# Optimization experiments

Hardware: AMD Instinct MI355X
Metric: run time of the kernel (lower is better)

## Reference

```python
import jax, jax.numpy as jnp
import numpy as np

HIDDEN = 512
NUM_HEADS = 4
EPS = 1e-12  # torch F.normalize eps


def setup_inputs() -> dict:
    key = jax.random.key(0)
    k1, k2, k3, k4 = jax.random.split(key, 4)
    B, N, C = 4, 8192, HIDDEN
    x = jax.random.normal(k1, (B, N, C), dtype=jnp.float32)
    # nn.Linear weights: stored as [out_features, in_features]
    s = 1.0 / np.sqrt(C)
    W_qkv = jax.random.uniform(k2, (3 * C, C), dtype=jnp.float32, minval=-s, maxval=s)
    W_out = jax.random.uniform(k3, (C, C), dtype=jnp.float32, minval=-s, maxval=s)
    b_out = jax.random.uniform(k4, (C,), dtype=jnp.float32, minval=-s, maxval=s)
    temperature = jnp.ones((NUM_HEADS, 1, 1), dtype=jnp.float32)
    return {
        "x": x, "W_qkv": W_qkv, "W_out": W_out, "b_out": b_out,
        "temperature": temperature,
        "B_in": B, "C_in": C, "H": 32, "W": 32, "D": 8,
    }


def _l2norm(t):
    # F.normalize(t, dim=-1): t / max(||t||_2, eps)
    n = jnp.sqrt(jnp.sum(t * t, axis=-1, keepdims=True))
    return t / jnp.maximum(n, EPS)


def reference(x, W_qkv, W_out, b_out, temperature, B_in, C_in, H, W, D):
    B, N, C = x.shape
    h = NUM_HEADS
    dh = C // h
    # qkv: [B, N, 3C] -> [3, B, h, N, dh]
    qkv = (x @ W_qkv.T).reshape(B, N, 3, h, dh).transpose(2, 0, 3, 1, 4)
    q, k, v = qkv[0], qkv[1], qkv[2]
    # transpose to channel-major: [B, h, dh, N]
    q = jnp.swapaxes(q, -2, -1)
    k = jnp.swapaxes(k, -2, -1)
    v = jnp.swapaxes(v, -2, -1)
    q = _l2norm(q)
    k = _l2norm(k)
    # cross-covariance attention over channels: [B, h, dh, dh]
    attn = jnp.einsum('bhcn,bhdn->bhcd', q, k) * temperature
    attn = jax.nn.softmax(attn, axis=-1)
    # [B, h, dh, N] -> [B, N, h, dh] -> [B, N, C]
    x_ca = jnp.einsum('bhcd,bhdn->bhcn', attn, v)
    x_ca = x_ca.transpose(0, 3, 1, 2).reshape(B, N, C)
    return x_ca @ W_out.T + b_out
```

## Files before the change

kernel.cpp:

```cpp
#include <hip/hip_runtime.h>


typedef unsigned short ushort_t;
typedef __attribute__((ext_vector_type(8))) short short8;
typedef __attribute__((ext_vector_type(4))) float float4v;
typedef __attribute__((ext_vector_type(4))) unsigned short ushort4v;

__device__ __forceinline__ float bf2f(ushort_t b) {
  union { unsigned u; float f; } c; c.u = ((unsigned)b) << 16; return c.f;
}
__device__ __forceinline__ ushort_t f2bf(float f) {
  union { float f; unsigned u; } c; c.f = f;
  unsigned u = c.u;
  u += 0x7fffu + ((u >> 16) & 1u);
  return (ushort_t)(u >> 16);
}

typedef const __attribute__((address_space(1))) unsigned int guint_t;
typedef __attribute__((address_space(3))) unsigned int luint_t;
__device__ __forceinline__ void gl_lds16(const ushort_t* g, ushort_t* l) {
  __builtin_amdgcn_global_load_lds((guint_t*)g, (luint_t*)l, 16, 0, 0);
}

__global__ __launch_bounds__(256) void convert_bf16(
    const float* __restrict__ x, const float* __restrict__ w1,
    const float* __restrict__ w2, ushort_t* __restrict__ xb,
    ushort_t* __restrict__ w1b, ushort_t* __restrict__ w2b) {
  int g = blockIdx.x * 256 + threadIdx.x;
  const float* src; ushort_t* dst; int off;
  if (g < 4194304)      { src = x;  dst = xb;  off = g; }
  else if (g < 4390912) { src = w1; dst = w1b; off = g - 4194304; }
  else                  { src = w2; dst = w2b; off = g - 4390912; }
  size_t e = (size_t)off * 4;
  float4v f = *(const float4v*)(src + e);
  ushort4v o;
#pragma unroll
  for (int i = 0; i < 4; ++i) o[i] = f2bf(f[i]);
  *(ushort4v*)(dst + e) = o;
}

template <int MODE>
__global__ __launch_bounds__(256) void gemm128(
    const ushort_t* __restrict__ A, const ushort_t* __restrict__ B,
    float* __restrict__ outF, ushort_t* __restrict__ outU,
    ushort_t* __restrict__ q_ws, ushort_t* __restrict__ k_ws,
    ushort_t* __restrict__ v_tok, const float* __restrict__ bias) {
  const int tid = threadIdx.x;
  const int z = blockIdx.z;
  const int n0 = blockIdx.x * 128;
  const int m0 = blockIdx.y * 128;

  int lda, ldb, K;
  const ushort_t *Ab, *Bb;
  if constexpr (MODE == 0) { lda = 512; ldb = 512; K = 512; Ab = A; Bb = B; }
  else if constexpr (MODE == 1) {
    int bh = z >> 3, s = z & 7;
    lda = 8192; ldb = 8192; K = 1024;
    Ab = A + (size_t)bh * 1048576 + s * 1024;
    Bb = B + (size_t)bh * 1048576 + s * 1024;
  } else if constexpr (MODE == 2) {
    lda = 512; ldb = 128; K = 128;
    Ab = A + (z & 3) * 128;
    Bb = B + (size_t)z * 16384;
  } else {
    lda = 512; ldb = 512; K = 512;
    Ab = A + (size_t)z * 8192 * 512;
    Bb = B + (size_t)z * 512 * 512;
  }

  __shared__ ushort_t sA[128 * 64];
  __shared__ ushort_t sB[128 * 64];

  const int lr = tid >> 3;
  const int lc = (tid & 7) * 8;
  const ushort_t* ga = Ab + (size_t)(m0 + lr) * lda + lc;
  const ushort_t* gb = Bb + (size_t)(n0 + lr) * ldb + lc;
  ushort_t* la = &sA[lr * 64 + lc];
  ushort_t* lb = &sB[lr * 64 + lc];
  const size_t aStep = (size_t)32 * lda;
  const size_t bStep = (size_t)32 * ldb;

  const int w = tid >> 6;
  const int lane = tid & 63;
  const int l15 = lane & 15;
  const int quad = lane >> 4;
  const int wm = (w >> 1) * 64, wn = (w & 1) * 64;

  float4v acc[4][4];
#pragma unroll
  for (int i = 0; i < 4; ++i)
#pragma unroll
    for (int j = 0; j < 4; ++j) acc[i][j] = (float4v){0.f, 0.f, 0.f, 0.f};

  for (int kk = 0; kk < K; kk += 64) {
    __syncthreads();
#pragma unroll
    for (int i = 0; i < 4; ++i) {
      gl_lds16(ga + i * aStep + kk, la + i * 2048);
      gl_lds16(gb + i * bStep + kk, lb + i * 2048);
    }
    __syncthreads();
#pragma unroll
    for (int k2 = 0; k2 < 64; k2 += 32) {
      short8 af[4], bfr[4];
#pragma unroll
      for (int i = 0; i < 4; ++i)
        af[i] = *(const short8*)&sA[(wm + i * 16 + l15) * 64 + k2 + quad * 8];
#pragma unroll
      for (int j = 0; j < 4; ++j)
        bfr[j] = *(const short8*)&sB[(wn + j * 16 + l15) * 64 + k2 + quad * 8];
#pragma unroll
      for (int i = 0; i < 4; ++i)
#pragma unroll
        for (int j = 0; j < 4; ++j)
          acc[i][j] = __builtin_amdgcn_mfma_f32_16x16x32_bf16(af[i], bfr[j], acc[i][j], 0, 0, 0);
    }
  }

  if constexpr (MODE == 0) {
    const int t3 = n0 >> 9;
    const int h = (n0 >> 7) & 3;
    if (t3 == 2) {
#pragma unroll
      for (int i = 0; i < 4; ++i)
#pragma unroll
        for (int j = 0; j < 4; ++j) {
          int col = wn + j * 16 + l15;
#pragma unroll
          for (int rg = 0; rg < 4; ++rg) {
            int gr = m0 + wm + i * 16 + quad * 4 + rg;
            int b = gr >> 13, n = gr & 8191;
            v_tok[((size_t)b * 8192 + n) * 512 + h * 128 + col] = f2bf(acc[i][j][rg]);
          }
        }
    } else {
      ushort_t* dstT = t3 ? k_ws : q_ws;
#pragma unroll
      for (int i = 0; i < 4; ++i) {
        int gr = m0 + wm + i * 16 + quad * 4;
        int b = gr >> 13, n = gr & 8191;
        int bh = b * 4 + h;
#pragma unroll
        for (int j = 0; j < 4; ++j) {
          ushort4v pk;
#pragma unroll
          for (int rg = 0; rg < 4; ++rg) pk[rg] = f2bf(acc[i][j][rg]);
          *(ushort4v*)(dstT + ((size_t)bh * 128 + (wn + j * 16 + l15)) * 8192 + n) = pk;
        }
      }
    }
  } else if constexpr (MODE == 1) {
#pragma unroll
    for (int i = 0; i < 4; ++i)
#pragma unroll
      for (int j = 0; j < 4; ++j)
#pragma unroll
        for (int rg = 0; rg < 4; ++rg)
          outF[(size_t)z * 16384 + (size_t)(wm + i * 16 + quad * 4 + rg) * 128 +
               wn + j * 16 + l15] = acc[i][j][rg];
  } else if constexpr (MODE == 2) {
    int b = z >> 2, h = z & 3;
#pragma unroll
    for (int i = 0; i < 4; ++i)
#pragma unroll
      for (int j = 0; j < 4; ++j)
#pragma unroll
        for (int rg = 0; rg < 4; ++rg)
          outU[((size_t)b * 512 + m0 + wm + i * 16 + quad * 4 + rg) * 512 +
               h * 128 + wn + j * 16 + l15] = f2bf(acc[i][j][rg]);
  } else {
#pragma unroll
    for (int i = 0; i < 4; ++i)
#pragma unroll
      for (int j = 0; j < 4; ++j) {
        int gcol = n0 + wn + j * 16 + l15;
        float bv = bias[gcol];
#pragma unroll
        for (int rg = 0; rg < 4; ++rg)
          outF[((size_t)z * 8192 + m0 + wm + i * 16 + quad * 4 + rg) * 512 + gcol] =
              acc[i][j][rg] + bv;
      }
  }
}

__global__ __launch_bounds__(256) void norms_kernel(
    const ushort_t* __restrict__ q, const ushort_t* __restrict__ k,
    float* __restrict__ norms) {
  int w = threadIdx.x >> 6, lane = threadIdx.x & 63;
  int idx = blockIdx.x * 4 + w;
  const ushort_t* p = ((idx >> 11) ? k : q) + (size_t)(idx & 2047) * 8192;
  float s = 0.f;
#pragma unroll
  for (int it = 0; it < 16; ++it) {
    short8 v = *(const short8*)(p + (size_t)(it * 64 + lane) * 8);
#pragma unroll
    for (int e = 0; e < 8; ++e) {
      float f = bf2f((ushort_t)v[e]);
      s += f * f;
    }
  }
#pragma unroll
  for (int off = 32; off; off >>= 1) s += __shfl_xor(s, off);
  if (lane == 0) norms[idx] = sqrtf(s);
}

__global__ void attn_softmax(const float* __restrict__ Sp,
                             const float* __restrict__ norms,
                             const float* __restrict__ temp,
                             ushort_t* __restrict__ attn_t) {
  int c = blockIdx.x, bh = blockIdx.y, h = bh & 3;
  int lane = threadIdx.x;
  const float* base = Sp + (size_t)bh * 8 * 16384 + (size_t)c * 128;
  float v0 = 0.f, v1 = 0.f;
#pragma unroll
  for (int s = 0; s < 8; ++s) {
    v0 += base[s * 16384 + lane];
    v1 += base[s * 16384 + lane + 64];
  }
  float nq = fmaxf(norms[bh * 128 + c], 1e-12f);
  float sc = temp[h] / nq;
  v0 = v0 * sc / fmaxf(norms[2048 + bh * 128 + lane], 1e-12f);
  v1 = v1 * sc / fmaxf(norms[2048 + bh * 128 + lane + 64], 1e-12f);
  float m = fmaxf(v0, v1);
#pragma unroll
  for (int off = 32; off; off >>= 1) m = fmaxf(m, __shfl_xor(m, off));
  float e0 = expf(v0 - m), e1 = expf(v1 - m);
  float s = e0 + e1;
#pragma unroll
  for (int off = 32; off; off >>= 1) s += __shfl_xor(s, off);
  float inv = 1.0f / s;
  attn_t[(size_t)bh * 16384 + (size_t)lane * 128 + c] = f2bf(e0 * inv);
  attn_t[(size_t)bh * 16384 + (size_t)(lane + 64) * 128 + c] = f2bf(e1 * inv);
}

extern "C" void kernel_launch(void* const* d_in, const int* in_sizes, int n_in,
                              void* d_out, int out_size, void* d_ws, size_t ws_size,
                              hipStream_t stream) {
  const float* x    = (const float*)d_in[0];
  const float* Wqkv = (const float*)d_in[1];
  const float* Wout = (const float*)d_in[2];
  const float* bout = (const float*)d_in[3];
  const float* temp = (const float*)d_in[4];
  float* out = (float*)d_out;

  char* ws = (char*)d_ws;
  ushort_t* x_bf  = (ushort_t*)(ws);
  float*    S_par = (float*)(ws);
  float*    norms = (float*)(ws + 8388608);
  ushort_t* attnT = (ushort_t*)(ws + 8404992);
  ushort_t* W2b   = (ushort_t*)(ws + 8929280);
  ushort_t* q_ws  = (ushort_t*)(ws + 33554432);
  ushort_t* k_ws  = (ushort_t*)(ws + 67108864);
  ushort_t* v_tok = (ushort_t*)(ws + 100663296);
  ushort_t* Wqkvb = (ushort_t*)(ws + 134217728);
  ushort_t* Woutb = (ushort_t*)(ws + 135790592);

  convert_bf16<<<dim3(17408), dim3(256), 0, stream>>>(x, Wqkv, Wout, x_bf, Wqkvb, Woutb);

  gemm128<0><<<dim3(12, 256, 1), dim3(256), 0, stream>>>(
      x_bf, Wqkvb, nullptr, nullptr, q_ws, k_ws, v_tok, nullptr);

  norms_kernel<<<dim3(1024), dim3(256), 0, stream>>>(q_ws, k_ws, norms);

  gemm128<1><<<dim3(1, 1, 128), dim3(256), 0, stream>>>(
      q_ws, k_ws, S_par, nullptr, nullptr, nullptr, nullptr, nullptr);

  attn_softmax<<<dim3(128, 16), dim3(64), 0, stream>>>(S_par, norms, temp, attnT);

  gemm128<2><<<dim3(1, 4, 16), dim3(256), 0, stream>>>(
      Woutb, attnT, nullptr, W2b, nullptr, nullptr, nullptr, nullptr);

  gemm128<3><<<dim3(4, 64, 4), dim3(256), 0, stream>>>(
      v_tok, W2b, out, nullptr, nullptr, nullptr, nullptr, bout);
}
```

Before: 302.7 us.

## Fuse x bf16 conversion and norm computation into QKV GEMM, remap grids for XCD locality

Drops the separate fp32-to-bf16 conversion of x and instead converts it in registers inside a new QKV GEMM kernel, with register prefetch of the next K slice. The squared L2 norms of q and k are accumulated in the GEMM epilogue with atomics, replacing the standalone norms kernel. V output uses a swapped MFMA operand order so token-major stores are vectorized. The split-K for the Gram GEMM doubles to 16 splits, and the QKV and output GEMMs use 1D grids remapped so blocks are grouped by XCD. In exchange it adds a memset, float atomics that make norm summation order nondeterministic, and more register pressure.

```diff
diff --git a/kernel.cpp b/kernel.cpp
--- a/kernel.cpp
+++ b/kernel.cpp
@@ -22,68 +22,195 @@
   __builtin_amdgcn_global_load_lds((guint_t*)g, (luint_t*)l, 16, 0, 0);
 }
 
-__global__ __launch_bounds__(256) void convert_bf16(
-    const float* __restrict__ x, const float* __restrict__ w1,
-    const float* __restrict__ w2, ushort_t* __restrict__ xb,
+__global__ __launch_bounds__(256) void convert_w(
+    const float* __restrict__ w1, const float* __restrict__ w2,
     ushort_t* __restrict__ w1b, ushort_t* __restrict__ w2b) {
   int g = blockIdx.x * 256 + threadIdx.x;
   const float* src; ushort_t* dst; int off;
-  if (g < 4194304)      { src = x;  dst = xb;  off = g; }
-  else if (g < 4390912) { src = w1; dst = w1b; off = g - 4194304; }
-  else                  { src = w2; dst = w2b; off = g - 4390912; }
+  if (g < 196608) { src = w1; dst = w1b; off = g; }
+  else            { src = w2; dst = w2b; off = g - 196608; }
   size_t e = (size_t)off * 4;
   float4v f = *(const float4v*)(src + e);
   ushort4v o;
 #pragma unroll
   for (int i = 0; i < 4; ++i) o[i] = f2bf(f[i]);
   *(ushort4v*)(dst + e) = o;
+}
+
+template <bool SWAP>
+__device__ __forceinline__ void qkv_kloop(
+    const float* ga, const ushort_t* gb, ushort_t* la, ushort_t* lb,
+    const ushort_t* sA, const ushort_t* sB,
+    float4v (&acc)[4][4], int wm, int wn, int l15, int quad) {
+  float4v a0[4], a1[4];
+#pragma unroll
+  for (int i = 0; i < 4; ++i) {
+    a0[i] = *(const float4v*)(ga + i * 16384);
+    a1[i] = *(const float4v*)(ga + i * 16384 + 4);
+  }
+#pragma unroll
+  for (int kk = 0; kk < 512; kk += 64) {
+    __syncthreads();
+#pragma unroll
+    for (int i = 0; i < 4; ++i) {
+      short8 cv;
+#pragma unroll
+      for (int e = 0; e < 4; ++e) {
+        cv[e]     = (short)f2bf(a0[i][e]);
+        cv[e + 4] = (short)f2bf(a1[i][e]);
+      }
+      *(short8*)(la + i * 2048) = cv;
+      gl_lds16(gb + i * 16384 + kk, lb + i * 2048);
+    }
+    __syncthreads();
+    if (kk < 448) {
+#pragma unroll
+      for (int i = 0; i < 4; ++i) {
+        a0[i] = *(const float4v*)(ga + i * 16384 + kk + 64);
+        a1[i] = *(const float4v*)(ga + i * 16384 + kk + 68);
+      }
+    }
+#pragma unroll
+    for (int k2 = 0; k2 < 64; k2 += 32) {
+      short8 af[4], bfr[4];
+#pragma unroll
+      for (int i = 0; i < 4; ++i)
+        af[i] = *(const short8*)&sA[(wm + i * 16 + l15) * 64 + k2 + quad * 8];
+#pragma unroll
+      for (int j = 0; j < 4; ++j)
+        bfr[j] = *(const short8*)&sB[(wn + j * 16 + l15) * 64 + k2 + quad * 8];
+#pragma unroll
+      for (int i = 0; i < 4; ++i)
+#pragma unroll
+        for (int j = 0; j < 4; ++j) {
+          if constexpr (SWAP)
+            acc[i][j] = __builtin_amdgcn_mfma_f32_16x16x32_bf16(bfr[j], af[i], acc[i][j], 0, 0, 0);
+          else
+            acc[i][j] = __builtin_amdgcn_mfma_f32_16x16x32_bf16(af[i], bfr[j], acc[i][j], 0, 0, 0);
+        }
+    }
+  }
+}
+
+__global__ __launch_bounds__(256) void qkv_kernel(
+    const float* __restrict__ x, const ushort_t* __restrict__ Wb,
+    ushort_t* __restrict__ q_ws, ushort_t* __restrict__ k_ws,
+    ushort_t* __restrict__ v_tok, float* __restrict__ normsSq) {
+  const int l = blockIdx.x;
+  const int xcd = l & 7, lx = l >> 3;
+  const int col = lx % 12;
+  const int mrow = xcd * 32 + lx / 12;
+  const int n0 = col * 128, m0 = mrow * 128;
+
+  __shared__ ushort_t sA[8192];
+  __shared__ ushort_t sB[8192];
+
+  const int tid = threadIdx.x;
+  const int lr = tid >> 3, lc = (tid & 7) * 8;
+  const float* ga = x + (size_t)(m0 + lr) * 512 + lc;
+  const ushort_t* gb = Wb + (size_t)(n0 + lr) * 512 + lc;
+  ushort_t* la = &sA[lr * 64 + lc];
+  ushort_t* lb = &sB[lr * 64 + lc];
+
+  const int w = tid >> 6, lane = tid & 63, l15 = lane & 15, quad = lane >> 4;
+  const int wm = (w >> 1) * 64, wn = (w & 1) * 64;
+
+  float4v acc[4][4];
+#pragma unroll
+  for (int i = 0; i < 4; ++i)
+#pragma unroll
+    for (int j = 0; j < 4; ++j) acc[i][j] = (float4v){0.f, 0.f, 0.f, 0.f};
+
+  const bool isV = (n0 >= 1024);
+  if (isV) qkv_kloop<true>(ga, gb, la, lb, sA, sB, acc, wm, wn, l15, quad);
+  else     qkv_kloop<false>(ga, gb, la, lb, sA, sB, acc, wm, wn, l15, quad);
+
+  const int b = m0 >> 13;
+  if (isV) {
+    const int chBase = n0 - 1024;
+#pragma unroll
+    for (int i = 0; i < 4; ++i) {
+      int tok = m0 + wm + i * 16 + l15;
+      int n = tok & 8191;
+      ushort_t* dst = v_tok + ((size_t)b * 8192 + n) * 512 + chBase + wn + quad * 4;
+#pragma unroll
+      for (int j = 0; j < 4; ++j) {
+        ushort4v pk;
+#pragma unroll
+        for (int rg = 0; rg < 4; ++rg) pk[rg] = f2bf(acc[i][j][rg]);
+        *(ushort4v*)(dst + j * 16) = pk;
+      }
+    }
+  } else {
+    const int t3 = n0 >> 9;
+    const int h = (n0 >> 7) & 3;
+    const int bh = b * 4 + h;
+    ushort_t* dstT = t3 ? k_ws : q_ws;
+    float* nrm = normsSq + (t3 ? 2048 : 0) + bh * 128;
+#pragma unroll
+    for (int j = 0; j < 4; ++j) {
+      int c = wn + j * 16 + l15;
+      float s = 0.f;
+#pragma unroll
+      for (int i = 0; i < 4; ++i) {
+        int n = (m0 + wm + i * 16 + quad * 4) & 8191;
+        ushort4v pk;
+#pragma unroll
+        for (int rg = 0; rg < 4; ++rg) {
+          float v = acc[i][j][rg];
+          pk[rg] = f2bf(v);
+          s += v * v;
+        }
+        *(ushort4v*)(dstT + ((size_t)bh * 128 + c) * 8192 + n) = pk;
+      }
+      s += __shfl_xor(s, 16);
+      s += __shfl_xor(s, 32);
+      if (quad == 0) atomicAdd(nrm + c, s);
+    }
+  }
 }
 
 template <int MODE>
 __global__ __launch_bounds__(256) void gemm128(
     const ushort_t* __restrict__ A, const ushort_t* __restrict__ B,
     float* __restrict__ outF, ushort_t* __restrict__ outU,
-    ushort_t* __restrict__ q_ws, ushort_t* __restrict__ k_ws,
-    ushort_t* __restrict__ v_tok, const float* __restrict__ bias) {
+    const float* __restrict__ bias) {
+  constexpr int K = (MODE == 2) ? 128 : 512;
   const int tid = threadIdx.x;
-  const int z = blockIdx.z;
-  const int n0 = blockIdx.x * 128;
-  const int m0 = blockIdx.y * 128;
-
-  int lda, ldb, K;
+  int z, m0, n0, lda, ldb;
   const ushort_t *Ab, *Bb;
-  if constexpr (MODE == 0) { lda = 512; ldb = 512; K = 512; Ab = A; Bb = B; }
-  else if constexpr (MODE == 1) {
-    int bh = z >> 3, s = z & 7;
-    lda = 8192; ldb = 8192; K = 1024;
-    Ab = A + (size_t)bh * 1048576 + s * 1024;
-    Bb = B + (size_t)bh * 1048576 + s * 1024;
+  if constexpr (MODE == 1) {
+    z = blockIdx.z;
+    int bh = z >> 4, s = z & 15;
+    m0 = 0; n0 = 0; lda = 8192; ldb = 8192;
+    Ab = A + (size_t)bh * 1048576 + s * 512;
+    Bb = B + (size_t)bh * 1048576 + s * 512;
   } else if constexpr (MODE == 2) {
-    lda = 512; ldb = 128; K = 128;
+    z = blockIdx.z;
+    m0 = blockIdx.y * 128; n0 = 0; lda = 512; ldb = 128;
     Ab = A + (z & 3) * 128;
     Bb = B + (size_t)z * 16384;
   } else {
-    lda = 512; ldb = 512; K = 512;
+    int l = blockIdx.x;
+    int xcd = l & 7, lx = l >> 3;
+    int colb = lx & 3;
+    int mr = xcd * 32 + (lx >> 2);
+    z = mr >> 6; m0 = (mr & 63) * 128; n0 = colb * 128;
+    lda = 512; ldb = 512;
     Ab = A + (size_t)z * 8192 * 512;
     Bb = B + (size_t)z * 512 * 512;
   }
 
-  __shared__ ushort_t sA[128 * 64];
-  __shared__ ushort_t sB[128 * 64];
-
-  const int lr = tid >> 3;
-  const int lc = (tid & 7) * 8;
+  __shared__ ushort_t sA[8192];
+  __shared__ ushort_t sB[8192];
+
+  const int lr = tid >> 3, lc = (tid & 7) * 8;
   const ushort_t* ga = Ab + (size_t)(m0 + lr) * lda + lc;
   const ushort_t* gb = Bb + (size_t)(n0 + lr) * ldb + lc;
   ushort_t* la = &sA[lr * 64 + lc];
   ushort_t* lb = &sB[lr * 64 + lc];
-  const size_t aStep = (size_t)32 * lda;
-  const size_t bStep = (size_t)32 * ldb;
-
-  const int w = tid >> 6;
-  const int lane = tid & 63;
-  const int l15 = lane & 15;
-  const int quad = lane >> 4;
+
+  const int w = tid >> 6, lane = tid & 63, l15 = lane & 15, quad = lane >> 4;
   const int wm = (w >> 1) * 64, wn = (w & 1) * 64;
 
   float4v acc[4][4];
@@ -92,12 +219,13 @@
 #pragma unroll
     for (int j = 0; j < 4; ++j) acc[i][j] = (float4v){0.f, 0.f, 0.f, 0.f};
 
+#pragma unroll
   for (int kk = 0; kk < K; kk += 64) {
     __syncthreads();
 #pragma unroll
     for (int i = 0; i < 4; ++i) {
-      gl_lds16(ga + i * aStep + kk, la + i * 2048);
-      gl_lds16(gb + i * bStep + kk, lb + i * 2048);
+      gl_lds16(ga + (size_t)i * 32 * lda + kk, la + i * 2048);
+      gl_lds16(gb + (size_t)i * 32 * ldb + kk, lb + i * 2048);
     }
     __syncthreads();
 #pragma unroll
@@ -117,39 +245,7 @@
     }
   }
 
-  if constexpr (MODE == 0) {
-    const int t3 = n0 >> 9;
-    const int h = (n0 >> 7) & 3;
-    if (t3 == 2) {
-#pragma unroll
-      for (int i = 0; i < 4; ++i)
-#pragma unroll
-        for (int j = 0; j < 4; ++j) {
-          int col = wn + j * 16 + l15;
-#pragma unroll
-          for (int rg = 0; rg < 4; ++rg) {
-            int gr = m0 + wm + i * 16 + quad * 4 + rg;
-            int b = gr >> 13, n = gr & 8191;
-            v_tok[((size_t)b * 8192 + n) * 512 + h * 128 + col] = f2bf(acc[i][j][rg]);
-          }
-        }
-    } else {
-      ushort_t* dstT = t3 ? k_ws : q_ws;
-#pragma unroll
-      for (int i = 0; i < 4; ++i) {
-        int gr = m0 + wm + i * 16 + quad * 4;
-        int b = gr >> 13, n = gr & 8191;
-        int bh = b * 4 + h;
-#pragma unroll
-        for (int j = 0; j < 4; ++j) {
-          ushort4v pk;
-#pragma unroll
-          for (int rg = 0; rg < 4; ++rg) pk[rg] = f2bf(acc[i][j][rg]);
-          *(ushort4v*)(dstT + ((size_t)bh * 128 + (wn + j * 16 + l15)) * 8192 + n) = pk;
-        }
-      }
-    }
-  } else if constexpr (MODE == 1) {
+  if constexpr (MODE == 1) {
 #pragma unroll
     for (int i = 0; i < 4; ++i)
 #pragma unroll
@@ -183,44 +279,23 @@
   }
 }
 
-__global__ __launch_bounds__(256) void norms_kernel(
-    const ushort_t* __restrict__ q, const ushort_t* __restrict__ k,
-    float* __restrict__ norms) {
-  int w = threadIdx.x >> 6, lane = threadIdx.x & 63;
-  int idx = blockIdx.x * 4 + w;
-  const ushort_t* p = ((idx >> 11) ? k : q) + (size_t)(idx & 2047) * 8192;
-  float s = 0.f;
-#pragma unroll
-  for (int it = 0; it < 16; ++it) {
-    short8 v = *(const short8*)(p + (size_t)(it * 64 + lane) * 8);
-#pragma unroll
-    for (int e = 0; e < 8; ++e) {
-      float f = bf2f((ushort_t)v[e]);
-      s += f * f;
-    }
-  }
-#pragma unroll
-  for (int off = 32; off; off >>= 1) s += __shfl_xor(s, off);
-  if (lane == 0) norms[idx] = sqrtf(s);
-}
-
 __global__ void attn_softmax(const float* __restrict__ Sp,
-                             const float* __restrict__ norms,
+                             const float* __restrict__ normsSq,
                              const float* __restrict__ temp,
                              ushort_t* __restrict__ attn_t) {
   int c = blockIdx.x, bh = blockIdx.y, h = bh & 3;
   int lane = threadIdx.x;
-  const float* base = Sp + (size_t)bh * 8 * 16384 + (size_t)c * 128;
+  const float* base = Sp + (size_t)bh * 16 * 16384 + (size_t)c * 128;
   float v0 = 0.f, v1 = 0.f;
 #pragma unroll
-  for (int s = 0; s < 8; ++s) {
+  for (int s = 0; s < 16; ++s) {
     v0 += base[s * 16384 + lane];
     v1 += base[s * 16384 + lane + 64];
   }
-  float nq = fmaxf(norms[bh * 128 + c], 1e-12f);
+  float nq = fmaxf(sqrtf(normsSq[bh * 128 + c]), 1e-12f);
   float sc = temp[h] / nq;
-  v0 = v0 * sc / fmaxf(norms[2048 + bh * 128 + lane], 1e-12f);
-  v1 = v1 * sc / fmaxf(norms[2048 + bh * 128 + lane + 64], 1e-12f);
+  v0 = v0 * sc / fmaxf(sqrtf(normsSq[2048 + bh * 128 + lane]), 1e-12f);
+  v1 = v1 * sc / fmaxf(sqrtf(normsSq[2048 + bh * 128 + lane + 64]), 1e-12f);
   float m = fmaxf(v0, v1);
 #pragma unroll
   for (int off = 32; off; off >>= 1) m = fmaxf(m, __shfl_xor(m, off));
@@ -244,32 +319,31 @@
   float* out = (float*)d_out;
 
   char* ws = (char*)d_ws;
-  ushort_t* x_bf  = (ushort_t*)(ws);
-  float*    S_par = (float*)(ws);
-  float*    norms = (float*)(ws + 8388608);
-  ushort_t* attnT = (ushort_t*)(ws + 8404992);
-  ushort_t* W2b   = (ushort_t*)(ws + 8929280);
-  ushort_t* q_ws  = (ushort_t*)(ws + 33554432);
-  ushort_t* k_ws  = (ushort_t*)(ws + 67108864);
-  ushort_t* v_tok = (ushort_t*)(ws + 100663296);
-  ushort_t* Wqkvb = (ushort_t*)(ws + 134217728);
-  ushort_t* Woutb = (ushort_t*)(ws + 135790592);
-
-  convert_bf16<<<dim3(17408), dim3(256), 0, stream>>>(x, Wqkv, Wout, x_bf, Wqkvb, Woutb);
-
-  gemm128<0><<<dim3(12, 256, 1), dim3(256), 0, stream>>>(
-      x_bf, Wqkvb, nullptr, nullptr, q_ws, k_ws, v_tok, nullptr);
-
-  norms_kernel<<<dim3(1024), dim3(256), 0, stream>>>(q_ws, k_ws, norms);
-
-  gemm128<1><<<dim3(1, 1, 128), dim3(256), 0, stream>>>(
-      q_ws, k_ws, S_par, nullptr, nullptr, nullptr, nullptr, nullptr);
-
-  attn_softmax<<<dim3(128, 16), dim3(64), 0, stream>>>(S_par, norms, temp, attnT);
+  float*    S_par   = (float*)(ws);
+  float*    normsSq = (float*)(ws + 16777216);
+  ushort_t* attnT   = (ushort_t*)(ws + 16793600);
+  ushort_t* W2b     = (ushort_t*)(ws + 17317888);
+  ushort_t* q_ws    = (ushort_t*)(ws + 33554432);
+  ushort_t* k_ws    = (ushort_t*)(ws + 67108864);
+  ushort_t* v_tok   = (ushort_t*)(ws + 100663296);
+  ushort_t* Wqkvb   = (ushort_t*)(ws + 134217728);
+  ushort_t* Woutb   = (ushort_t*)(ws + 135790592);
+
+  hipMemsetAsync(normsSq, 0, 16384, stream);
+
+  convert_w<<<dim3(1024), dim3(256), 0, stream>>>(Wqkv, Wout, Wqkvb, Woutb);
+
+  qkv_kernel<<<dim3(3072), dim3(256), 0, stream>>>(
+      x, Wqkvb, q_ws, k_ws, v_tok, normsSq);
+
+  gemm128<1><<<dim3(1, 1, 256), dim3(256), 0, stream>>>(
+      q_ws, k_ws, S_par, nullptr, nullptr);
+
+  attn_softmax<<<dim3(128, 16), dim3(64), 0, stream>>>(S_par, normsSq, temp, attnT);
 
   gemm128<2><<<dim3(1, 4, 16), dim3(256), 0, stream>>>(
-      Woutb, attnT, nullptr, W2b, nullptr, nullptr, nullptr, nullptr);
-
-  gemm128<3><<<dim3(4, 64, 4), dim3(256), 0, stream>>>(
-      v_tok, W2b, out, nullptr, nullptr, nullptr, nullptr, bout);
-}
+      Woutb, attnT, nullptr, W2b, nullptr);
+
+  gemm128<3><<<dim3(1024), dim3(256), 0, stream>>>(
+      v_tok, W2b, out, nullptr, bout);
+}
```

New measurement: 332.3 us. 9.8% more time.
